# Performance work log

Hardware: AMD Instinct MI355X
Metric: run time of the kernel (lower is better)

## Reference

```python
import jax, jax.numpy as jnp
import numpy as np

B, T, IN, H, P = 1024, 100, 1, 256, 0.5


def _lstm_scan(xs, h0, c0, Wih, Whh, bih, bhh, mask_h, mask_in=None):
    """Run an LSTMCell over time with variational dropout masks.
    xs: [T, B, D]. mask_h multiplies the recurrent hidden state (as in the
    original: cell(x_t, (h * mask1, c))); mask_in (optional) multiplies input.
    PyTorch LSTMCell gate order: i, f, g, o."""
    b = bih + bhh

    def step(carry, xt):
        h, c = carry
        xin = xt if mask_in is None else xt * mask_in
        g = xin @ Wih.T + (h * mask_h) @ Whh.T + b  # [B, 4H]
        i, f, gg, o = jnp.split(g, 4, axis=-1)
        c = jax.nn.sigmoid(f) * c + jax.nn.sigmoid(i) * jnp.tanh(gg)
        h = jax.nn.sigmoid(o) * jnp.tanh(c)
        return (h, c), h

    _, hs = jax.lax.scan(step, (h0, c0), xs)
    return hs  # [T, B, H]


def setup_inputs() -> dict:
    key = jax.random.key(0)
    ks = jax.random.split(key, 24)
    s = 1.0 / np.sqrt(H)

    def u(k, shape):
        return jax.random.uniform(k, shape, jnp.float32, -s, s)

    inp = {"x0": jax.random.normal(ks[0], (B, T, IN), jnp.float32)}
    names = ["1f", "1b", "2f", "2b"]
    in_sizes = [2 * IN, 2 * IN, 2 * H, 2 * H]
    i = 1
    for n, d in zip(names, in_sizes):
        inp[f"Wih{n}"] = u(ks[i], (4 * H, d)); i += 1
        inp[f"Whh{n}"] = u(ks[i], (4 * H, H)); i += 1
        inp[f"bih{n}"] = u(ks[i], (4 * H,)); i += 1
        inp[f"bhh{n}"] = u(ks[i], (4 * H,)); i += 1
    inp["Wout"] = u(ks[17], (IN, 2 * H))
    inp["bout"] = u(ks[18], (IN,))
    # Variational dropout masks (Bernoulli(1 - dropout_prob)), per set_dropout(batch)
    def bern(k, shape):
        return (jax.random.uniform(k, shape) > P).astype(jnp.float32)
    inp["mask1"] = bern(ks[19], (B, H))
    inp["mask2"] = bern(ks[20], (B, 2 * H))
    inp["mask3"] = bern(ks[21], (B, H))
    inp["mask4"] = bern(ks[22], (B, 1, 2 * H))
    return inp


def reference(x0,
              Wih1f, Whh1f, bih1f, bhh1f,
              Wih1b, Whh1b, bih1b, bhh1b,
              Wih2f, Whh2f, bih2f, bhh2f,
              Wih2b, Whh2b, bih2b, bhh2b,
              Wout, bout, mask1, mask2, mask3, mask4):
    batch = x0.shape[0]
    m = x0.mean(axis=1, keepdims=True)                       # [B, 1, IN]
    x = jnp.concatenate([x0 - m, jnp.broadcast_to(m, x0.shape)], axis=2)  # [B, T, 2*IN]
    xs = jnp.swapaxes(x, 0, 1)                               # [T, B, 2*IN]

    h0 = jnp.zeros((batch, H), x0.dtype)
    c0 = jnp.zeros((batch, H), x0.dtype)

    # Layer 1, forward and backward in time (backward outputs NOT re-flipped,
    # faithful to the original which stacks them in reversed-visit order).
    hf = _lstm_scan(xs, h0, c0, Wih1f, Whh1f, bih1f, bhh1f, mask1)
    hb = _lstm_scan(xs[::-1], h0, c0, Wih1b, Whh1b, bih1b, bhh1b, mask1)
    p1 = jnp.concatenate([hf, hb], axis=-1)                  # [T, B, 2H]

    # Layer 2 with input mask2 and recurrent mask3
    h2f = _lstm_scan(p1, h0, c0, Wih2f, Whh2f, bih2f, bhh2f, mask3, mask_in=mask2)
    h2b = _lstm_scan(p1[::-1], h0, c0, Wih2b, Whh2b, bih2b, bhh2b, mask3, mask_in=mask2)
    p2 = jnp.concatenate([h2f, h2b], axis=-1)                # [T, B, 2H]

    pa = jnp.swapaxes(p2, 0, 1)                              # [B, T, 2H]
    pred = (pa * mask4) @ Wout.T + bout                      # [B, T, IN]
    return pred + m
```

## Files before the change

### kernel.cpp

```cpp
#include <hip/hip_runtime.h>
#include <cstdint>
#include <cstddef>

#define B_  1024
#define T_  100
#define H_  256

typedef _Float16 f16x8 __attribute__((ext_vector_type(8)));
typedef float    f32x16 __attribute__((ext_vector_type(16)));

__device__ __forceinline__ float sigm(float x){ return 1.0f/(1.0f + __expf(-x)); }
__device__ __forceinline__ float tanh_(float x){ return 1.0f - 2.0f/(1.0f + __expf(2.0f*x)); }

#define W_WHH1F 0
#define W_WHH1B 262144
#define W_WIH2F 524288
#define W_WIH2B 1048576
#define W_WHH2F 1572864
#define W_WHH2B 1835008
#define W_TOTAL 2097152

__device__ __forceinline__ void gemm_chunk(
    f32x16 acc[4],
    const _Float16* __restrict__ Asrc, int a_stride,
    const _Float16* __restrict__ Wsrc, int w_stride,
    _Float16* Alds,
    int b0, int j0, int lane, int rw, int cw)
{
  const int t = threadIdx.x;
  #pragma unroll
  for (int i = 0; i < 8; i++){
    int u   = t + 256*i;
    int row = u >> 5;
    int c8  = u & 31;
    uint4 v = *(const uint4*)(Asrc + (size_t)(b0 + row)*a_stride + c8*8);
    *(uint4*)(Alds + row*264 + c8*8) = v;
  }
  __syncthreads();
  const _Float16* arow = Alds + (rw*32 + (lane & 31))*264 + (lane >> 5)*8;
  const int nbase = j0 + cw*32 + (lane & 31);
  const int kq    = (lane >> 5)*8;
  #pragma unroll
  for (int kk = 0; kk < 16; kk++){
    f16x8 a = *(const f16x8*)(arow + kk*16);
    #pragma unroll
    for (int g = 0; g < 4; g++){
      const _Float16* wp = Wsrc + (size_t)(g*256 + nbase)*w_stride + kk*16 + kq;
      f16x8 bw = *(const f16x8*)wp;
      acc[g] = __builtin_amdgcn_mfma_f32_32x32x16_f16(a, bw, acc[g], 0, 0, 0);
    }
  }
  __syncthreads();
}

__global__ void conv_weights(const float* __restrict__ Whh1f, const float* __restrict__ Whh1b,
                             const float* __restrict__ Wih2f, const float* __restrict__ Wih2b,
                             const float* __restrict__ Whh2f, const float* __restrict__ Whh2b,
                             _Float16* __restrict__ dst)
{
  int idx = blockIdx.x*256 + threadIdx.x;
  if      (idx < W_WHH1B) dst[idx] = (_Float16)Whh1f[idx];
  else if (idx < W_WIH2F) dst[idx] = (_Float16)Whh1b[idx - W_WHH1B];
  else if (idx < W_WIH2B) dst[idx] = (_Float16)Wih2f[idx - W_WIH2F];
  else if (idx < W_WHH2F) dst[idx] = (_Float16)Wih2b[idx - W_WIH2B];
  else if (idx < W_WHH2B) dst[idx] = (_Float16)Whh2f[idx - W_WHH2F];
  else if (idx < W_TOTAL) dst[idx] = (_Float16)Whh2b[idx - W_WHH2B];
}

__global__ __launch_bounds__(256, 2)
void l1_step(const _Float16* __restrict__ wpool,
             const float* __restrict__ Wih_f,
             const float* __restrict__ Wih_b,
             const float* __restrict__ bih_f,
             const float* __restrict__ bhh_f,
             const float* __restrict__ bih_b,
             const float* __restrict__ bhh_b,
             const float* __restrict__ x0,
             const float* __restrict__ mvec,
             const float* __restrict__ mask1,
             const float* __restrict__ mask2,
             const _Float16* __restrict__ hm_in,
             _Float16* __restrict__ hm_out,
             float* __restrict__ cbuf,
             _Float16* __restrict__ p1m,
             int s)
{
  __shared__ __align__(16) _Float16 Alds[64*264];
  const int dir = blockIdx.z;
  const int b0  = blockIdx.x*64, j0 = blockIdx.y*64;
  const int lane = threadIdx.x & 63;
  const int w = threadIdx.x >> 6, rw = w >> 1, cw = w & 1;

  f32x16 acc[4];
  #pragma unroll
  for (int g = 0; g < 4; g++)
    #pragma unroll
    for (int e = 0; e < 16; e++) acc[g][e] = 0.0f;

  const _Float16* Whh = wpool + (dir ? W_WHH1B : W_WHH1F);
  gemm_chunk(acc, hm_in + (size_t)dir*B_*H_, H_, Whh, H_, Alds, b0, j0, lane, rw, cw);

  const int tin = dir ? (T_-1-s) : s;
  const float* Wih = dir ? Wih_b : Wih_f;
  const float* bih = dir ? bih_b : bih_f;
  const float* bhh = dir ? bhh_b : bhh_f;
  const int jj = j0 + cw*32 + (lane & 31);

  float wi0[4], wi1[4], bs[4];
  #pragma unroll
  for (int g = 0; g < 4; g++){
    int n = g*256 + jj;
    wi0[g] = Wih[n*2 + 0];
    wi1[g] = Wih[n*2 + 1];
    bs[g]  = bih[n] + bhh[n];
  }
  float* cp = cbuf + (size_t)dir*B_*H_;
  _Float16* hmo = hm_out + (size_t)dir*B_*H_;

  #pragma unroll
  for (int r = 0; r < 16; r++){
    int row = (r & 3) + 8*(r >> 2) + 4*(lane >> 5);
    int b   = b0 + rw*32 + row;
    float mv = mvec[b];
    float xd = x0[b*T_ + tin] - mv;
    float gi = acc[0][r] + xd*wi0[0] + mv*wi1[0] + bs[0];
    float gf = acc[1][r] + xd*wi0[1] + mv*wi1[1] + bs[1];
    float gg = acc[2][r] + xd*wi0[2] + mv*wi1[2] + bs[2];
    float go = acc[3][r] + xd*wi0[3] + mv*wi1[3] + bs[3];
    float ii = sigm(gi), ff = sigm(gf), g2 = tanh_(gg), oo = sigm(go);
    size_t cidx = (size_t)b*H_ + jj;
    float cn = ff*cp[cidx] + ii*g2;
    cp[cidx] = cn;
    float h = oo*tanh_(cn);
    hmo[cidx] = (_Float16)(h * mask1[cidx]);
    p1m[((size_t)s*B_ + b)*512 + dir*256 + jj] =
        (_Float16)(h * mask2[(size_t)b*512 + dir*256 + jj]);
  }
}

__global__ __launch_bounds__(256, 2)
void l2_step(const _Float16* __restrict__ wpool,
             const float* __restrict__ bih_f,
             const float* __restrict__ bhh_f,
             const float* __restrict__ bih_b,
             const float* __restrict__ bhh_b,
             const _Float16* __restrict__ p1m,
             const float* __restrict__ mask3,
             const float* __restrict__ mask4,
             const float* __restrict__ Wout,
             const _Float16* __restrict__ hm_in,
             _Float16* __restrict__ hm_out,
             float* __restrict__ cbuf,
             float* __restrict__ pred,
             int s)
{
  __shared__ __align__(16) _Float16 Alds[64*264];
  const int dir = blockIdx.z;
  const int b0  = blockIdx.x*64, j0 = blockIdx.y*64;
  const int lane = threadIdx.x & 63;
  const int w = threadIdx.x >> 6, rw = w >> 1, cw = w & 1;

  f32x16 acc[4];
  #pragma unroll
  for (int g = 0; g < 4; g++)
    #pragma unroll
    for (int e = 0; e < 16; e++) acc[g][e] = 0.0f;

  const int tin = dir ? (T_-1-s) : s;
  const _Float16* Wih = wpool + (dir ? W_WIH2B : W_WIH2F);
  const _Float16* Whh = wpool + (dir ? W_WHH2B : W_WHH2F);
  const _Float16* Ain = p1m + (size_t)tin*B_*512;

  gemm_chunk(acc, Ain,       512, Wih,       512, Alds, b0, j0, lane, rw, cw);
  gemm_chunk(acc, Ain + 256, 512, Wih + 256, 512, Alds, b0, j0, lane, rw, cw);
  gemm_chunk(acc, hm_in + (size_t)dir*B_*H_, H_, Whh, H_, Alds, b0, j0, lane, rw, cw);

  const float* bih = dir ? bih_b : bih_f;
  const float* bhh = dir ? bhh_b : bhh_f;
  const int jj = j0 + cw*32 + (lane & 31);
  float bs[4];
  #pragma unroll
  for (int g = 0; g < 4; g++)
    bs[g] = bih[g*256 + jj] + bhh[g*256 + jj];
  float wo = Wout[dir*256 + jj];
  float* cp = cbuf + (size_t)dir*B_*H_;
  _Float16* hmo = hm_out + (size_t)dir*B_*H_;

  #pragma unroll
  for (int r = 0; r < 16; r++){
    int row = (r & 3) + 8*(r >> 2) + 4*(lane >> 5);
    int b   = b0 + rw*32 + row;
    float gi = acc[0][r] + bs[0];
    float gf = acc[1][r] + bs[1];
    float gg = acc[2][r] + bs[2];
    float go = acc[3][r] + bs[3];
    float ii = sigm(gi), ff = sigm(gf), g2 = tanh_(gg), oo = sigm(go);
    size_t cidx = (size_t)b*H_ + jj;
    float cn = ff*cp[cidx] + ii*g2;
    cp[cidx] = cn;
    float h = oo*tanh_(cn);
    hmo[cidx] = (_Float16)(h * mask3[cidx]);
    float contrib = h * mask4[(size_t)b*512 + dir*256 + jj] * wo;
    contrib += __shfl_xor(contrib, 16);
    contrib += __shfl_xor(contrib, 8);
    contrib += __shfl_xor(contrib, 4);
    contrib += __shfl_xor(contrib, 2);
    contrib += __shfl_xor(contrib, 1);
    if ((lane & 31) == 0) atomicAdd(&pred[(size_t)b*T_ + s], contrib);
  }
}

__global__ void prep_kernel(const float* __restrict__ x0,
                            float* __restrict__ mvec)
{
  int b = blockIdx.x*blockDim.x + threadIdx.x;
  if (b < B_){
    float ssum = 0.0f;
    for (int t = 0; t < T_; t++) ssum += x0[b*T_ + t];
    mvec[b] = ssum * (1.0f / T_);
  }
}

__global__ void final_kernel(const float* __restrict__ pred,
                             const float* __restrict__ mvec,
                             const float* __restrict__ bout,
                             float* __restrict__ out)
{
  int idx = blockIdx.x*256 + threadIdx.x;
  if (idx < B_*T_){
    int b = idx / T_;
    out[idx] = pred[idx] + bout[0] + mvec[b];
  }
}

extern "C" void kernel_launch(void* const* d_in, const int* in_sizes, int n_in,
                              void* d_out, int out_size, void* d_ws, size_t ws_size,
                              hipStream_t stream)
{
  (void)in_sizes; (void)n_in; (void)out_size; (void)ws_size;
  const float* x0    = (const float*)d_in[0];
  const float* Wih1f = (const float*)d_in[1];
  const float* Whh1f = (const float*)d_in[2];
  const float* bih1f = (const float*)d_in[3];
  const float* bhh1f = (const float*)d_in[4];
  const float* Wih1b = (const float*)d_in[5];
  const float* Whh1b = (const float*)d_in[6];
  const float* bih1b = (const float*)d_in[7];
  const float* bhh1b = (const float*)d_in[8];
  const float* Wih2f = (const float*)d_in[9];
  const float* Whh2f = (const float*)d_in[10];
  const float* bih2f = (const float*)d_in[11];
  const float* bhh2f = (const float*)d_in[12];
  const float* Wih2b = (const float*)d_in[13];
  const float* Whh2b = (const float*)d_in[14];
  const float* bih2b = (const float*)d_in[15];
  const float* bhh2b = (const float*)d_in[16];
  const float* Wout  = (const float*)d_in[17];
  const float* bout  = (const float*)d_in[18];
  const float* mask1 = (const float*)d_in[19];
  const float* mask2 = (const float*)d_in[20];
  const float* mask3 = (const float*)d_in[21];
  const float* mask4 = (const float*)d_in[22];
  float* out = (float*)d_out;

  char* ws = (char*)d_ws;
  size_t off = 0;
  _Float16* wpool = (_Float16*)(ws + off); off += (size_t)W_TOTAL*2;
  _Float16* p1m  = (_Float16*)(ws + off); off += (size_t)T_*B_*512*2;
  float* pred = (float*)(ws + off); off += (size_t)B_*T_*4;
  float* mvec = (float*)(ws + off); off += (size_t)B_*4;
  float* cbuf = (float*)(ws + off); off += (size_t)2*2*B_*H_*4;
  _Float16* hm = (_Float16*)(ws + off); off += (size_t)2*2*2*B_*H_*2;

  hipMemsetAsync(pred, 0, (size_t)B_*T_*4, stream);
  hipMemsetAsync(cbuf, 0, (size_t)2*2*B_*H_*4 + (size_t)2*2*2*B_*H_*2, stream);

  conv_weights<<<dim3(W_TOTAL/256), dim3(256), 0, stream>>>(
      Whh1f, Whh1b, Wih2f, Wih2b, Whh2f, Whh2b, wpool);
  prep_kernel<<<dim3(4), dim3(256), 0, stream>>>(x0, mvec);

  dim3 grid(16, 4, 2), blk(256);
  float* cL1 = cbuf;
  float* cL2 = cbuf + (size_t)2*B_*H_;
  _Float16* hmL1 = hm;
  _Float16* hmL2 = hm + (size_t)2*2*B_*H_;
  const size_t pp = (size_t)2*B_*H_;

  for (int s = 0; s < T_; s++){
    l1_step<<<grid, blk, 0, stream>>>(wpool, Wih1f, Wih1b,
        bih1f, bhh1f, bih1b, bhh1b, x0, mvec, mask1, mask2,
        hmL1 + (size_t)(s & 1)*pp, hmL1 + (size_t)((s + 1) & 1)*pp, cL1, p1m, s);
  }
  for (int s = 0; s < T_; s++){
    l2_step<<<grid, blk, 0, stream>>>(wpool,
        bih2f, bhh2f, bih2b, bhh2b, p1m, mask3, mask4, Wout,
        hmL2 + (size_t)(s & 1)*pp, hmL2 + (size_t)((s + 1) & 1)*pp, cL2, pred, s);
  }
  final_kernel<<<dim3((B_*T_ + 255)/256), dim3(256), 0, stream>>>(pred, mvec, bout, out);
}
```

Baseline: 5.245 ms.

## Run each LSTM layer as one persistent kernel with batch-sliced blocks

Replaces 200 per-timestep launches with two persistent kernels. Each block owns 32 batch rows for all 256 hidden units of one direction, so the recurrence needs no inter-block synchronisation. Hidden state stays in LDS and cell state in registers, which removes the global h/c round trips and per-step launch overhead. Weights are prepacked into an MFMA-fragment order so B-operand loads are contiguous. In exchange only 64 blocks run on a large GPU, each streaming the full Whh (and Wih for layer 2) every step from L2, which leaves most CUs idle.

Measured after the change: 6.003 ms. 14.5% more time.

```diff
diff --git a/kernel.cpp b/kernel.cpp
--- a/kernel.cpp
+++ b/kernel.cpp
@@ -20,198 +20,212 @@
 #define W_WHH2B 1835008
 #define W_TOTAL 2097152
 
-__device__ __forceinline__ void gemm_chunk(
-    f32x16 acc[4],
-    const _Float16* __restrict__ Asrc, int a_stride,
-    const _Float16* __restrict__ Wsrc, int w_stride,
-    _Float16* Alds,
-    int b0, int j0, int lane, int rw, int cw)
-{
-  const int t = threadIdx.x;
-  #pragma unroll
-  for (int i = 0; i < 8; i++){
-    int u   = t + 256*i;
-    int row = u >> 5;
-    int c8  = u & 31;
-    uint4 v = *(const uint4*)(Asrc + (size_t)(b0 + row)*a_stride + c8*8);
-    *(uint4*)(Alds + row*264 + c8*8) = v;
-  }
-  __syncthreads();
-  const _Float16* arow = Alds + (rw*32 + (lane & 31))*264 + (lane >> 5)*8;
-  const int nbase = j0 + cw*32 + (lane & 31);
-  const int kq    = (lane >> 5)*8;
-  #pragma unroll
-  for (int kk = 0; kk < 16; kk++){
-    f16x8 a = *(const f16x8*)(arow + kk*16);
-    #pragma unroll
-    for (int g = 0; g < 4; g++){
-      const _Float16* wp = Wsrc + (size_t)(g*256 + nbase)*w_stride + kk*16 + kq;
-      f16x8 bw = *(const f16x8*)wp;
-      acc[g] = __builtin_amdgcn_mfma_f32_32x32x16_f16(a, bw, acc[g], 0, 0, 0);
-    }
-  }
-  __syncthreads();
-}
-
-__global__ void conv_weights(const float* __restrict__ Whh1f, const float* __restrict__ Whh1b,
+__global__ void pack_weights(const float* __restrict__ Whh1f, const float* __restrict__ Whh1b,
                              const float* __restrict__ Wih2f, const float* __restrict__ Wih2b,
                              const float* __restrict__ Whh2f, const float* __restrict__ Whh2b,
                              _Float16* __restrict__ dst)
 {
-  int idx = blockIdx.x*256 + threadIdx.x;
-  if      (idx < W_WHH1B) dst[idx] = (_Float16)Whh1f[idx];
-  else if (idx < W_WIH2F) dst[idx] = (_Float16)Whh1b[idx - W_WHH1B];
-  else if (idx < W_WIH2B) dst[idx] = (_Float16)Wih2f[idx - W_WIH2F];
-  else if (idx < W_WHH2F) dst[idx] = (_Float16)Wih2b[idx - W_WIH2B];
-  else if (idx < W_WHH2B) dst[idx] = (_Float16)Whh2f[idx - W_WHH2F];
-  else if (idx < W_TOTAL) dst[idx] = (_Float16)Whh2b[idx - W_WHH2B];
-}
-
-__global__ __launch_bounds__(256, 2)
-void l1_step(const _Float16* __restrict__ wpool,
-             const float* __restrict__ Wih_f,
-             const float* __restrict__ Wih_b,
-             const float* __restrict__ bih_f,
-             const float* __restrict__ bhh_f,
-             const float* __restrict__ bih_b,
-             const float* __restrict__ bhh_b,
-             const float* __restrict__ x0,
-             const float* __restrict__ mvec,
-             const float* __restrict__ mask1,
-             const float* __restrict__ mask2,
-             const _Float16* __restrict__ hm_in,
-             _Float16* __restrict__ hm_out,
-             float* __restrict__ cbuf,
-             _Float16* __restrict__ p1m,
-             int s)
-{
-  __shared__ __align__(16) _Float16 Alds[64*264];
-  const int dir = blockIdx.z;
-  const int b0  = blockIdx.x*64, j0 = blockIdx.y*64;
-  const int lane = threadIdx.x & 63;
-  const int w = threadIdx.x >> 6, rw = w >> 1, cw = w & 1;
-
-  f32x16 acc[4];
-  #pragma unroll
-  for (int g = 0; g < 4; g++)
-    #pragma unroll
-    for (int e = 0; e < 16; e++) acc[g][e] = 0.0f;
-
-  const _Float16* Whh = wpool + (dir ? W_WHH1B : W_WHH1F);
-  gemm_chunk(acc, hm_in + (size_t)dir*B_*H_, H_, Whh, H_, Alds, b0, j0, lane, rw, cw);
-
-  const int tin = dir ? (T_-1-s) : s;
+  int fid = blockIdx.x*256 + threadIdx.x;
+  const float* src; int base, nkk, ksh, lf;
+  if      (fid <  32768){ src=Whh1f; base=W_WHH1F; nkk=16; ksh=4; lf=fid; }
+  else if (fid <  65536){ src=Whh1b; base=W_WHH1B; nkk=16; ksh=4; lf=fid-32768; }
+  else if (fid < 131072){ src=Wih2f; base=W_WIH2F; nkk=32; ksh=5; lf=fid-65536; }
+  else if (fid < 196608){ src=Wih2b; base=W_WIH2B; nkk=32; ksh=5; lf=fid-131072; }
+  else if (fid < 229376){ src=Whh2f; base=W_WHH2F; nkk=16; ksh=4; lf=fid-196608; }
+  else                  { src=Whh2b; base=W_WHH2B; nkk=16; ksh=4; lf=fid-229376; }
+  int l  = lf & 63;
+  int t  = lf >> 6;
+  int kk = t & (nkk-1);
+  int r  = t >> ksh;
+  int g  = r & 3, cc = r >> 2;
+  int K  = nkk*16;
+  int n  = g*256 + cc*32 + (l & 31);
+  int k  = kk*16 + ((l >> 5) << 3);
+  const float4* s4 = (const float4*)(src + (size_t)n*K + k);
+  float4 v0 = s4[0], v1 = s4[1];
+  f16x8 o;
+  o[0]=(_Float16)v0.x; o[1]=(_Float16)v0.y; o[2]=(_Float16)v0.z; o[3]=(_Float16)v0.w;
+  o[4]=(_Float16)v1.x; o[5]=(_Float16)v1.y; o[6]=(_Float16)v1.z; o[7]=(_Float16)v1.w;
+  *(f16x8*)(dst + (size_t)base + (size_t)lf*8) = o;
+}
+
+__global__ __launch_bounds__(512, 2)
+void l1_phase(const _Float16* __restrict__ wpool,
+              const float* __restrict__ Wih_f, const float* __restrict__ Wih_b,
+              const float* __restrict__ bih_f, const float* __restrict__ bhh_f,
+              const float* __restrict__ bih_b, const float* __restrict__ bhh_b,
+              const float* __restrict__ x0, const float* __restrict__ mvec,
+              const float* __restrict__ mask1, const float* __restrict__ mask2,
+              _Float16* __restrict__ p1m)
+{
+  __shared__ __align__(16) _Float16 hlds[8192];
+  const int bid = blockIdx.x;
+  const int dir = bid >> 5, rc = bid & 31;
+  const int tid = threadIdx.x, lane = tid & 63, w = tid >> 6;
+  const int b0 = rc*32;
+  const int hcol = w*32 + (lane & 31);
+  const _Float16* whh = wpool + (dir ? W_WHH1B : W_WHH1F);
+
+  #pragma unroll
+  for (int i = 0; i < 16; i++) hlds[tid + 512*i] = (_Float16)0.f;
+
   const float* Wih = dir ? Wih_b : Wih_f;
   const float* bih = dir ? bih_b : bih_f;
   const float* bhh = dir ? bhh_b : bhh_f;
-  const int jj = j0 + cw*32 + (lane & 31);
-
   float wi0[4], wi1[4], bs[4];
   #pragma unroll
   for (int g = 0; g < 4; g++){
-    int n = g*256 + jj;
-    wi0[g] = Wih[n*2 + 0];
-    wi1[g] = Wih[n*2 + 1];
+    int n = g*256 + hcol;
+    wi0[g] = Wih[n*2]; wi1[g] = Wih[n*2 + 1];
     bs[g]  = bih[n] + bhh[n];
   }
-  float* cp = cbuf + (size_t)dir*B_*H_;
-  _Float16* hmo = hm_out + (size_t)dir*B_*H_;
-
+  int rowv[16]; float m1v[16], m2v[16], mvv[16], creg[16];
   #pragma unroll
   for (int r = 0; r < 16; r++){
     int row = (r & 3) + 8*(r >> 2) + 4*(lane >> 5);
-    int b   = b0 + rw*32 + row;
-    float mv = mvec[b];
-    float xd = x0[b*T_ + tin] - mv;
-    float gi = acc[0][r] + xd*wi0[0] + mv*wi1[0] + bs[0];
-    float gf = acc[1][r] + xd*wi0[1] + mv*wi1[1] + bs[1];
-    float gg = acc[2][r] + xd*wi0[2] + mv*wi1[2] + bs[2];
-    float go = acc[3][r] + xd*wi0[3] + mv*wi1[3] + bs[3];
-    float ii = sigm(gi), ff = sigm(gf), g2 = tanh_(gg), oo = sigm(go);
-    size_t cidx = (size_t)b*H_ + jj;
-    float cn = ff*cp[cidx] + ii*g2;
-    cp[cidx] = cn;
-    float h = oo*tanh_(cn);
-    hmo[cidx] = (_Float16)(h * mask1[cidx]);
-    p1m[((size_t)s*B_ + b)*512 + dir*256 + jj] =
-        (_Float16)(h * mask2[(size_t)b*512 + dir*256 + jj]);
-  }
-}
-
-__global__ __launch_bounds__(256, 2)
-void l2_step(const _Float16* __restrict__ wpool,
-             const float* __restrict__ bih_f,
-             const float* __restrict__ bhh_f,
-             const float* __restrict__ bih_b,
-             const float* __restrict__ bhh_b,
-             const _Float16* __restrict__ p1m,
-             const float* __restrict__ mask3,
-             const float* __restrict__ mask4,
-             const float* __restrict__ Wout,
-             const _Float16* __restrict__ hm_in,
-             _Float16* __restrict__ hm_out,
-             float* __restrict__ cbuf,
-             float* __restrict__ pred,
-             int s)
-{
-  __shared__ __align__(16) _Float16 Alds[64*264];
-  const int dir = blockIdx.z;
-  const int b0  = blockIdx.x*64, j0 = blockIdx.y*64;
-  const int lane = threadIdx.x & 63;
-  const int w = threadIdx.x >> 6, rw = w >> 1, cw = w & 1;
-
-  f32x16 acc[4];
-  #pragma unroll
-  for (int g = 0; g < 4; g++)
-    #pragma unroll
-    for (int e = 0; e < 16; e++) acc[g][e] = 0.0f;
-
-  const int tin = dir ? (T_-1-s) : s;
-  const _Float16* Wih = wpool + (dir ? W_WIH2B : W_WIH2F);
-  const _Float16* Whh = wpool + (dir ? W_WHH2B : W_WHH2F);
-  const _Float16* Ain = p1m + (size_t)tin*B_*512;
-
-  gemm_chunk(acc, Ain,       512, Wih,       512, Alds, b0, j0, lane, rw, cw);
-  gemm_chunk(acc, Ain + 256, 512, Wih + 256, 512, Alds, b0, j0, lane, rw, cw);
-  gemm_chunk(acc, hm_in + (size_t)dir*B_*H_, H_, Whh, H_, Alds, b0, j0, lane, rw, cw);
+    rowv[r] = row;
+    int b = b0 + row;
+    m1v[r] = mask1[(size_t)b*H_ + hcol];
+    m2v[r] = mask2[(size_t)b*512 + dir*256 + hcol];
+    mvv[r] = mvec[b];
+    creg[r] = 0.0f;
+  }
+  const int wbase = (hcol >> 4)*512 + ((hcol >> 3) & 1)*256 + (hcol & 7);
+  __syncthreads();
+
+  for (int s = 0; s < T_; s++){
+    const int tin = dir ? (T_-1-s) : s;
+    f32x16 acc[4];
+    #pragma unroll
+    for (int g = 0; g < 4; g++)
+      #pragma unroll
+      for (int e = 0; e < 16; e++) acc[g][e] = 0.0f;
+
+    #pragma unroll 4
+    for (int kk = 0; kk < 16; kk++){
+      f16x8 a = *(const f16x8*)(hlds + kk*512 + lane*8);
+      #pragma unroll
+      for (int g = 0; g < 4; g++){
+        f16x8 bw = *(const f16x8*)(whh + (size_t)(((w*4 + g)*16 + kk)*512 + lane*8));
+        acc[g] = __builtin_amdgcn_mfma_f32_32x32x16_f16(a, bw, acc[g], 0, 0, 0);
+      }
+    }
+    __syncthreads();
+
+    #pragma unroll
+    for (int r = 0; r < 16; r++){
+      int b = b0 + rowv[r];
+      float mv = mvv[r];
+      float xd = x0[b*T_ + tin] - mv;
+      float gi = acc[0][r] + xd*wi0[0] + mv*wi1[0] + bs[0];
+      float gf = acc[1][r] + xd*wi0[1] + mv*wi1[1] + bs[1];
+      float gg = acc[2][r] + xd*wi0[2] + mv*wi1[2] + bs[2];
+      float go = acc[3][r] + xd*wi0[3] + mv*wi1[3] + bs[3];
+      float ii = sigm(gi), ff = sigm(gf), g2 = tanh_(gg), oo = sigm(go);
+      float cn = ff*creg[r] + ii*g2;
+      creg[r] = cn;
+      float h = oo*tanh_(cn);
+      hlds[wbase + rowv[r]*8] = (_Float16)(h * m1v[r]);
+      p1m[((size_t)s*B_ + b)*512 + dir*256 + hcol] = (_Float16)(h * m2v[r]);
+    }
+    __syncthreads();
+  }
+}
+
+__global__ __launch_bounds__(512, 2)
+void l2_phase(const _Float16* __restrict__ wpool,
+              const float* __restrict__ bih_f, const float* __restrict__ bhh_f,
+              const float* __restrict__ bih_b, const float* __restrict__ bhh_b,
+              const _Float16* __restrict__ p1m,
+              const float* __restrict__ mask3, const float* __restrict__ mask4,
+              const float* __restrict__ Wout,
+              float* __restrict__ pred)
+{
+  __shared__ __align__(16) _Float16 hlds[8192];
+  const int bid = blockIdx.x;
+  const int dir = bid >> 5, rc = bid & 31;
+  const int tid = threadIdx.x, lane = tid & 63, w = tid >> 6;
+  const int b0 = rc*32;
+  const int hcol = w*32 + (lane & 31);
+  const _Float16* whh = wpool + (dir ? W_WHH2B : W_WHH2F);
+  const _Float16* wih = wpool + (dir ? W_WIH2B : W_WIH2F);
+
+  #pragma unroll
+  for (int i = 0; i < 16; i++) hlds[tid + 512*i] = (_Float16)0.f;
 
   const float* bih = dir ? bih_b : bih_f;
   const float* bhh = dir ? bhh_b : bhh_f;
-  const int jj = j0 + cw*32 + (lane & 31);
   float bs[4];
   #pragma unroll
-  for (int g = 0; g < 4; g++)
-    bs[g] = bih[g*256 + jj] + bhh[g*256 + jj];
-  float wo = Wout[dir*256 + jj];
-  float* cp = cbuf + (size_t)dir*B_*H_;
-  _Float16* hmo = hm_out + (size_t)dir*B_*H_;
-
+  for (int g = 0; g < 4; g++) bs[g] = bih[g*256 + hcol] + bhh[g*256 + hcol];
+  float wo = Wout[dir*256 + hcol];
+  int rowv[16]; float m3v[16], m4v[16], creg[16];
   #pragma unroll
   for (int r = 0; r < 16; r++){
     int row = (r & 3) + 8*(r >> 2) + 4*(lane >> 5);
-    int b   = b0 + rw*32 + row;
-    float gi = acc[0][r] + bs[0];
-    float gf = acc[1][r] + bs[1];
-    float gg = acc[2][r] + bs[2];
-    float go = acc[3][r] + bs[3];
-    float ii = sigm(gi), ff = sigm(gf), g2 = tanh_(gg), oo = sigm(go);
-    size_t cidx = (size_t)b*H_ + jj;
-    float cn = ff*cp[cidx] + ii*g2;
-    cp[cidx] = cn;
-    float h = oo*tanh_(cn);
-    hmo[cidx] = (_Float16)(h * mask3[cidx]);
-    float contrib = h * mask4[(size_t)b*512 + dir*256 + jj] * wo;
-    contrib += __shfl_xor(contrib, 16);
-    contrib += __shfl_xor(contrib, 8);
-    contrib += __shfl_xor(contrib, 4);
-    contrib += __shfl_xor(contrib, 2);
-    contrib += __shfl_xor(contrib, 1);
-    if ((lane & 31) == 0) atomicAdd(&pred[(size_t)b*T_ + s], contrib);
-  }
-}
-
-__global__ void prep_kernel(const float* __restrict__ x0,
-                            float* __restrict__ mvec)
+    rowv[r] = row;
+    int b = b0 + row;
+    m3v[r] = mask3[(size_t)b*H_ + hcol];
+    m4v[r] = mask4[(size_t)b*512 + dir*256 + hcol] * wo;
+    creg[r] = 0.0f;
+  }
+  const int wbase = (hcol >> 4)*512 + ((hcol >> 3) & 1)*256 + (hcol & 7);
+  __syncthreads();
+
+  for (int s = 0; s < T_; s++){
+    const int tin = dir ? (T_-1-s) : s;
+    f32x16 acc[4];
+    #pragma unroll
+    for (int g = 0; g < 4; g++)
+      #pragma unroll
+      for (int e = 0; e < 16; e++) acc[g][e] = 0.0f;
+
+    #pragma unroll 4
+    for (int kk = 0; kk < 16; kk++){
+      f16x8 a = *(const f16x8*)(hlds + kk*512 + lane*8);
+      #pragma unroll
+      for (int g = 0; g < 4; g++){
+        f16x8 bw = *(const f16x8*)(whh + (size_t)(((w*4 + g)*16 + kk)*512 + lane*8));
+        acc[g] = __builtin_amdgcn_mfma_f32_32x32x16_f16(a, bw, acc[g], 0, 0, 0);
+      }
+    }
+    const _Float16* arow2 = p1m + ((size_t)tin*B_ + b0 + (lane & 31))*512 + ((lane >> 5) << 3);
+    #pragma unroll 4
+    for (int kk = 0; kk < 32; kk++){
+      f16x8 a = *(const f16x8*)(arow2 + kk*16);
+      #pragma unroll
+      for (int g = 0; g < 4; g++){
+        f16x8 bw = *(const f16x8*)(wih + (size_t)(((w*4 + g)*32 + kk)*512 + lane*8));
+        acc[g] = __builtin_amdgcn_mfma_f32_32x32x16_f16(a, bw, acc[g], 0, 0, 0);
+      }
+    }
+    __syncthreads();
+
+    #pragma unroll
+    for (int r = 0; r < 16; r++){
+      int b = b0 + rowv[r];
+      float gi = acc[0][r] + bs[0];
+      float gf = acc[1][r] + bs[1];
+      float gg = acc[2][r] + bs[2];
+      float go = acc[3][r] + bs[3];
+      float ii = sigm(gi), ff = sigm(gf), g2 = tanh_(gg), oo = sigm(go);
+      float cn = ff*creg[r] + ii*g2;
+      creg[r] = cn;
+      float h = oo*tanh_(cn);
+      hlds[wbase + rowv[r]*8] = (_Float16)(h * m3v[r]);
+      float contrib = h * m4v[r];
+      contrib += __shfl_xor(contrib, 16);
+      contrib += __shfl_xor(contrib, 8);
+      contrib += __shfl_xor(contrib, 4);
+      contrib += __shfl_xor(contrib, 2);
+      contrib += __shfl_xor(contrib, 1);
+      if ((lane & 31) == 0) atomicAdd(&pred[(size_t)b*T_ + s], contrib);
+    }
+    __syncthreads();
+  }
+}
+
+__global__ void prep_kernel(const float* __restrict__ x0, float* __restrict__ mvec)
 {
   int b = blockIdx.x*blockDim.x + threadIdx.x;
   if (b < B_){
@@ -266,35 +280,19 @@
   char* ws = (char*)d_ws;
   size_t off = 0;
   _Float16* wpool = (_Float16*)(ws + off); off += (size_t)W_TOTAL*2;
-  _Float16* p1m  = (_Float16*)(ws + off); off += (size_t)T_*B_*512*2;
+  _Float16* p1m   = (_Float16*)(ws + off); off += (size_t)T_*B_*512*2;
   float* pred = (float*)(ws + off); off += (size_t)B_*T_*4;
-  float* mvec = (float*)(ws + off); off += (size_t)B_*4;
-  float* cbuf = (float*)(ws + off); off += (size_t)2*2*B_*H_*4;
-  _Float16* hm = (_Float16*)(ws + off); off += (size_t)2*2*2*B_*H_*2;
+  float* mvec = (float*)(ws + off); off += 4096;
 
   hipMemsetAsync(pred, 0, (size_t)B_*T_*4, stream);
-  hipMemsetAsync(cbuf, 0, (size_t)2*2*B_*H_*4 + (size_t)2*2*2*B_*H_*2, stream);
-
-  conv_weights<<<dim3(W_TOTAL/256), dim3(256), 0, stream>>>(
+
+  pack_weights<<<dim3(1024), dim3(256), 0, stream>>>(
       Whh1f, Whh1b, Wih2f, Wih2b, Whh2f, Whh2b, wpool);
   prep_kernel<<<dim3(4), dim3(256), 0, stream>>>(x0, mvec);
 
-  dim3 grid(16, 4, 2), blk(256);
-  float* cL1 = cbuf;
-  float* cL2 = cbuf + (size_t)2*B_*H_;
-  _Float16* hmL1 = hm;
-  _Float16* hmL2 = hm + (size_t)2*2*B_*H_;
-  const size_t pp = (size_t)2*B_*H_;
-
-  for (int s = 0; s < T_; s++){
-    l1_step<<<grid, blk, 0, stream>>>(wpool, Wih1f, Wih1b,
-        bih1f, bhh1f, bih1b, bhh1b, x0, mvec, mask1, mask2,
-        hmL1 + (size_t)(s & 1)*pp, hmL1 + (size_t)((s + 1) & 1)*pp, cL1, p1m, s);
-  }
-  for (int s = 0; s < T_; s++){
-    l2_step<<<grid, blk, 0, stream>>>(wpool,
-        bih2f, bhh2f, bih2b, bhh2b, p1m, mask3, mask4, Wout,
-        hmL2 + (size_t)(s & 1)*pp, hmL2 + (size_t)((s + 1) & 1)*pp, cL2, pred, s);
-  }
+  l1_phase<<<dim3(64), dim3(512), 0, stream>>>(wpool, Wih1f, Wih1b,
+      bih1f, bhh1f, bih1b, bhh1b, x0, mvec, mask1, mask2, p1m);
+  l2_phase<<<dim3(64), dim3(512), 0, stream>>>(wpool, bih2f, bhh2f,
+      bih2b, bhh2b, p1m, mask3, mask4, Wout, pred);
   final_kernel<<<dim3((B_*T_ + 255)/256), dim3(256), 0, stream>>>(pred, mvec, bout, out);
 }
```
